# Kernel tuning notes

Hardware: AMD Instinct MI355X
Metric: run time of the kernel (lower is better)

The kernel has to match this reference:

```python
import jax, jax.numpy as jnp
import numpy as np

# sarModule stage: in=256, out=512, blocks=2, stride=2, patch_groups=4, mask_size=7
B, C_IN, H, W = 32, 256, 56, 56
C_OUT = 512
PLANES = C_OUT // 4   # Bottleneck inner width = planes // expansion = 128
G = 4                 # patch_groups
MS = 7                # mask_size
TEMP = 1.0            # gumbel-softmax temperature


def conv(x, w, stride=1, pad=0, groups=1):
    return jax.lax.conv_general_dilated(
        x, w, (stride, stride), [(pad, pad), (pad, pad)],
        feature_group_count=groups,
        dimension_numbers=('NCHW', 'OIHW', 'NCHW'))


def bn(x, g, b):
    # BatchNorm in inference form with running_mean=0, running_var=1 folded in
    return x * g[None, :, None, None] + b[None, :, None, None]


def avgpool3s2(x):
    # nn.AvgPool2d(3, stride=2, padding=1), count_include_pad=True
    s = jax.lax.reduce_window(x, 0.0, jax.lax.add, (1, 1, 3, 3), (1, 1, 2, 2),
                              [(0, 0), (0, 0), (1, 1), (1, 1)])
    return s / 9.0


def setup_inputs() -> dict:
    key = jax.random.key(0)
    ks = iter(jax.random.split(key, 64))

    def w(shape):
        fan_in = int(np.prod(shape[1:]))
        return jax.random.normal(next(ks), shape, jnp.float32) * np.float32((2.0 / fan_in) ** 0.5)

    ones = lambda n: jnp.ones((n,), jnp.float32)
    zeros = lambda n: jnp.zeros((n,), jnp.float32)

    x = jax.random.normal(next(ks), (B, C_IN, H, W), jnp.float32)
    u = jax.random.uniform(next(ks), (B, 2, G, MS, MS), jnp.float32, 1e-6, 1.0 - 1e-6)
    gumbel_noise = -jnp.log(-jnp.log(u))

    return dict(
        x=x, gumbel_noise=gumbel_noise,
        # base Bottleneck (256->512, stride 2, downsample = avgpool + 1x1 conv + bn)
        b_w1=w((PLANES, C_IN, 1, 1)), b_g1=ones(PLANES), b_b1=zeros(PLANES),
        b_w2=w((PLANES, PLANES, 3, 3)), b_g2=ones(PLANES), b_b2=zeros(PLANES),
        b_w3=w((C_OUT, PLANES, 1, 1)), b_g3=ones(C_OUT), b_b3=zeros(C_OUT),
        b_dw=w((C_OUT, C_IN, 1, 1)), b_dg=ones(C_OUT), b_db=zeros(C_OUT),
        # refine Bottleneck (256->512, stride 1, downsample = 1x1 conv + bn)
        r_w1=w((PLANES, C_IN, 1, 1)), r_g1=ones(PLANES), r_b1=zeros(PLANES),
        r_w2=w((PLANES, PLANES, 3, 3)), r_g2=ones(PLANES), r_b2=zeros(PLANES),
        r_w3=w((C_OUT, PLANES, 1, 1)), r_g3=ones(C_OUT), r_b3=zeros(C_OUT),
        r_dw=w((C_OUT, C_IN, 1, 1)), r_dg=ones(C_OUT), r_db=zeros(C_OUT),
        # maskGen: grouped 3x3 conv (512 -> 4*G), bn, pool, grouped 1x1 fc (4*G -> 2*G)
        m_w=w((4 * G, C_OUT // G, 3, 3)), m_g=ones(4 * G), m_b=zeros(4 * G),
        m_fcw=w((2 * G, 4, 1, 1)),
        m_fcb=jnp.concatenate([0.1 * ones(G), 5.0 * ones(G)]),  # bias init from maskGen
        # fusion Bottleneck (512->512, stride 2, downsample = avgpool only)
        f_w1=w((PLANES, C_OUT, 1, 1)), f_g1=ones(PLANES), f_b1=zeros(PLANES),
        f_w2=w((PLANES, PLANES, 3, 3)), f_g2=ones(PLANES), f_b2=zeros(PLANES),
        f_w3=w((C_OUT, PLANES, 1, 1)), f_g3=ones(C_OUT), f_b3=zeros(C_OUT),
    )


def reference(x, gumbel_noise,
              b_w1, b_g1, b_b1, b_w2, b_g2, b_b2, b_w3, b_g3, b_b3, b_dw, b_dg, b_db,
              r_w1, r_g1, r_b1, r_w2, r_g2, r_b2, r_w3, r_g3, r_b3, r_dw, r_dg, r_db,
              m_w, m_g, m_b, m_fcw, m_fcb,
              f_w1, f_g1, f_b1, f_w2, f_g2, f_b2, f_w3, f_g3, f_b3):
    # ---- base branch: Bottleneck stride 2, last_relu=False -> [B,512,28,28]
    o = jax.nn.relu(bn(conv(x, b_w1), b_g1, b_b1))
    o = jax.nn.relu(bn(conv(o, b_w2, stride=2, pad=1), b_g2, b_b2))
    o = bn(conv(o, b_w3), b_g3, b_b3)
    x_base = o + bn(conv(avgpool3s2(x), b_dw), b_dg, b_db)

    # ---- maskGen on x_base
    gmap = jax.nn.relu(bn(conv(x_base, m_w, pad=1, groups=G), m_g, m_b))      # [B,16,28,28]
    hb = x_base.shape[2] // MS                                                 # adaptive avgpool 28->7
    gmap = gmap.reshape(B, 4 * G, MS, hb, MS, hb).mean(axis=(3, 5))            # [B,16,7,7]
    logits = conv(gmap, m_fcw, groups=G) + m_fcb[None, :, None, None]          # [B,8,7,7]
    logits = logits.reshape(B, 2, G, MS, MS)                                   # view(B,2,groups,ms,ms)
    # hard gumbel-softmax over dim 1 with straight-through estimator
    y = jax.nn.softmax((logits + gumbel_noise) / TEMP, axis=1)
    hard = jax.nn.one_hot(jnp.argmax(y, axis=1), 2, axis=1, dtype=y.dtype)
    gates = hard + y - jax.lax.stop_gradient(y)
    mask = gates[:, 1]                                                         # [B,G,7,7]

    # nearest-upsample mask x8 and expand across each channel group
    mask_up = jnp.repeat(jnp.repeat(mask, H // MS, axis=-2), W // MS, axis=-1) # [B,G,56,56]
    mask_full = jnp.broadcast_to(mask_up[:, :, None], (B, G, C_OUT // G, H, W)).reshape(B, C_OUT, H, W)

    # ---- refine branch: Bottleneck stride 1, output gated by mask, last_relu=False
    o = jax.nn.relu(bn(conv(x, r_w1), r_g1, r_b1))
    o = jax.nn.relu(bn(conv(o, r_w2, pad=1), r_g2, r_b2))
    o = bn(conv(o, r_w3), r_g3, r_b3) * mask_full
    x_refine = o + bn(conv(x, r_dw), r_dg, r_db)                               # [B,512,56,56]

    # ---- fuse: bilinear upsample base to refine resolution (align_corners=False)
    x_base_up = jax.image.resize(x_base, (B, C_OUT, H, W), 'bilinear')
    fused = jax.nn.relu(x_base_up + x_refine)

    # ---- fusion Bottleneck: stride 2, downsample = avgpool only, last_relu=True
    o = jax.nn.relu(bn(conv(fused, f_w1), f_g1, f_b1))
    o = jax.nn.relu(bn(conv(o, f_w2, stride=2, pad=1), f_g2, f_b2))
    o = bn(conv(o, f_w3), f_g3, f_b3)
    out = jax.nn.relu(o + avgpool3s2(fused))                                   # [B,512,28,28]
    return out, mask
```

## Files before the change

kernel.cpp:

```cpp
#include <hip/hip_runtime.h>
#include <cstdint>

#define BB   32
#define CINX 256
#define HH   56
#define WW   56
#define HWX  3136
#define CO   512
#define PL   128
#define HP   28
#define WP   28
#define HWP  784
#define NG   4
#define MSZ  7

typedef unsigned short ushortT;
typedef unsigned int   uint32;
typedef __attribute__((ext_vector_type(8))) short short8;
typedef __attribute__((ext_vector_type(4))) float f32x4;

__device__ __forceinline__ ushortT f2bf(float f){
  uint32 u = __float_as_uint(f);
  u = (u + 0x7fffu + ((u >> 16) & 1u)) >> 16;
  return (ushortT)u;
}
__device__ __forceinline__ float bf2f(ushortT u){
  return __uint_as_float(((uint32)u) << 16);
}
__device__ __forceinline__ void split2(float v, ushortT& h, ushortT& lo){
  h = f2bf(v);
  lo = f2bf(v - bf2f(h));
}
__device__ __forceinline__ uint32 packu(ushortT a, ushortT b){
  return (uint32)a | ((uint32)b << 16);
}

__device__ __forceinline__ void wsplit(float v, ushortT* dh, ushortT* dl, size_t i){
  ushortT h, lo; split2(v, h, lo); dh[i] = h; dl[i] = lo;
}

__global__ __launch_bounds__(256) void prep_w(
  const float* __restrict__ b_w1, const float* __restrict__ b_g1,
  const float* __restrict__ b_w2, const float* __restrict__ b_g2,
  const float* __restrict__ b_w3, const float* __restrict__ b_g3,
  const float* __restrict__ b_dw, const float* __restrict__ b_dg,
  const float* __restrict__ r_w1, const float* __restrict__ r_g1,
  const float* __restrict__ r_w2, const float* __restrict__ r_g2,
  const float* __restrict__ r_w3, const float* __restrict__ r_g3,
  const float* __restrict__ r_dw, const float* __restrict__ r_dg,
  const float* __restrict__ f_w1, const float* __restrict__ f_g1,
  const float* __restrict__ f_w2, const float* __restrict__ f_g2,
  const float* __restrict__ f_w3, const float* __restrict__ f_g3,
  ushortT* __restrict__ dh, ushortT* __restrict__ dl)
{
  const int idx = blockIdx.x*256 + threadIdx.x;
  switch (blockIdx.y){
    case 0: {
      if (idx >= 32768) return; int m = idx >> 8;
      wsplit(b_w1[idx]*b_g1[m], dh, dl, (size_t)0 + idx); } break;
    case 1: {
      if (idx >= 147456) return; int m = idx / 1152; int k = idx - m*1152;
      int tap = k >> 7, c = k & 127;
      wsplit(b_w2[((size_t)(m*128 + c))*9 + tap]*b_g2[m], dh, dl, 32768 + (size_t)idx); } break;
    case 2: {
      if (idx >= 196608) return; int m = idx / 384; int k = idx - m*384;
      float v = (k < 128) ? b_w3[m*128 + k]*b_g3[m] : b_dw[m*256 + (k-128)]*b_dg[m];
      wsplit(v, dh, dl, 180224 + (size_t)idx); } break;
    case 3: {
      if (idx >= 32768) return; int m = idx >> 8;
      wsplit(r_w1[idx]*r_g1[m], dh, dl, 376832 + (size_t)idx); } break;
    case 4: {
      if (idx >= 147456) return; int m = idx / 1152; int k = idx - m*1152;
      int tap = k >> 7, c = k & 127;
      wsplit(r_w2[((size_t)(m*128 + c))*9 + tap]*r_g2[m], dh, dl, 409600 + (size_t)idx); } break;
    case 5: {
      if (idx >= 196608) return; int m = idx / 384; int k = idx - m*384;
      float v = (k < 128) ? r_w3[m*128 + k]*r_g3[m] : r_dw[m*256 + (k-128)]*r_dg[m];
      wsplit(v, dh, dl, 557056 + (size_t)idx); } break;
    case 6: {
      if (idx >= 65536) return; int m = idx >> 9;
      wsplit(f_w1[idx]*f_g1[m], dh, dl, 753664 + (size_t)idx); } break;
    case 7: {
      if (idx >= 147456) return; int m = idx / 1152; int k = idx - m*1152;
      int tap = k >> 7, c = k & 127;
      wsplit(f_w2[((size_t)(m*128 + c))*9 + tap]*f_g2[m], dh, dl, 819200 + (size_t)idx); } break;
    case 8: {
      if (idx >= 65536) return; int m = idx >> 7;
      wsplit(f_w3[idx]*f_g3[m], dh, dl, 966656 + (size_t)idx); } break;
  }
}

__global__ __launch_bounds__(256) void k_avgpool_x(const float* __restrict__ x, float* __restrict__ out){
  int idx = blockIdx.x*256 + threadIdx.x;
  if (idx >= BB*CINX*HWP) return;
  int p = idx % HWP; int bc = idx / HWP;
  int ox = p % WP, oy = p / WP;
  const float* src = x + (size_t)bc*HWX;
  float s = 0.f;
  #pragma unroll
  for (int dy=0; dy<3; dy++){
    int yy = 2*oy-1+dy;
    if ((unsigned)yy >= HH) continue;
    #pragma unroll
    for (int dx=0; dx<3; dx++){
      int xx = 2*ox-1+dx;
      if ((unsigned)xx >= WW) continue;
      s += src[yy*WW + xx];
    }
  }
  out[idx] = s * (1.f/9.f);
}

__global__ __launch_bounds__(256) void prep_p(const float* __restrict__ t,
    ushortT* __restrict__ ph_, ushortT* __restrict__ pl_){
  __shared__ float s[16][17];
  const int p0 = blockIdx.x*16, c0 = blockIdx.y*16, bz = blockIdx.z;
  const int ci = threadIdx.x >> 4, pi = threadIdx.x & 15;
  s[ci][pi] = t[((size_t)bz*CINX + c0 + ci)*HWP + p0 + pi];
  __syncthreads();
  const int pr = threadIdx.x >> 4, cj = threadIdx.x & 15;
  float v = s[cj][pr];
  ushortT h, lo; split2(v, h, lo);
  size_t o = ((size_t)bz*HWP + p0 + pr)*CINX + c0 + cj;
  ph_[o] = h; pl_[o] = lo;
}

__global__ __launch_bounds__(256) void k_poolf(const ushortT* __restrict__ fzh,
    const ushortT* __restrict__ fzl, float* __restrict__ pf){
  const int p = blockIdx.x, bz = blockIdx.y;
  const int oy = p / WP, ox = p - oy*WP;
  const int c = threadIdx.x*2;
  float s0 = 0.f, s1 = 0.f;
  #pragma unroll
  for (int dy=0; dy<3; dy++){
    const int iy = 2*oy - 1 + dy;
    if ((unsigned)iy >= (unsigned)HH) continue;
    #pragma unroll
    for (int dx=0; dx<3; dx++){
      const int ix = 2*ox - 1 + dx;
      if ((unsigned)ix >= (unsigned)WW) continue;
      const size_t fi = ((size_t)bz*HWX + (size_t)(iy*WW + ix))*CO + c;
      uint32 hh = *(const uint32*)(fzh + fi);
      uint32 ll = *(const uint32*)(fzl + fi);
      s0 += bf2f((ushortT)(hh & 0xffff)) + bf2f((ushortT)(ll & 0xffff));
      s1 += bf2f((ushortT)(hh >> 16))    + bf2f((ushortT)(ll >> 16));
    }
  }
  const size_t o = ((size_t)bz*HWP + p)*CO + c;
  pf[o]   = s0 * (1.f/9.f);
  pf[o+1] = s1 * (1.f/9.f);
}

template<int KIND,int EPI,int S1F,int S2F,int STRIDE,int PAD,int HIN,int WIN,
         int WOUT,int NOUT,int C1,int C2,int MTOT,int KTOT>
__global__ __launch_bounds__(256)
void gemm_bf3(const ushortT* __restrict__ wph, const ushortT* __restrict__ wpl,
              const ushortT* __restrict__ s1h, const ushortT* __restrict__ s1l,
              const ushortT* __restrict__ s2h, const ushortT* __restrict__ s2l,
              const float* __restrict__ xf32,
              const float* __restrict__ bias1, const float* __restrict__ bias2,
              const float* __restrict__ maskf, const float* __restrict__ xbase,
              ushortT* __restrict__ oh, ushortT* __restrict__ ol,
              float* __restrict__ of32)
{
  __shared__ ushortT smem[16384];
  ushortT* AH  = smem;
  ushortT* AL  = smem + 4096;
  ushortT* BHs = smem + 8192;
  ushortT* BLs = smem + 12288;

  const int tid = threadIdx.x;
  const int nt = blockIdx.x, mt = blockIdx.y, bz = blockIdx.z;
  const int l  = tid & 63, w = tid >> 6;
  const int wm = w >> 1, wn = w & 1;

  const int sr = tid >> 1;
  const int hp = tid & 1;
  const int swz = (sr >> 1) & 3;
  const int lws0 = sr*32 + ((2*hp) ^ swz)*8;
  const int lws1 = sr*32 + ((2*hp + 1) ^ swz)*8;

  const size_t arow = (size_t)(mt*128 + sr)*KTOT + hp*16;

  const int ng = nt*128 + sr;
  int oyS = 0, oxS = 0;
  if (KIND == 1){ oyS = ng / WOUT; oxS = ng - (ng / WOUT)*WOUT; }

  float mvstage = 1.f;
  if (KIND == 3){
    if (ng < NOUT){
      int yy = ng / WOUT, xx = ng - (ng / WOUT)*WOUT;
      mvstage = maskf[((size_t)(bz*NG + mt)*MSZ + (yy>>3))*MSZ + (xx>>3)];
    } else mvstage = 0.f;
  }

  f32x4 acc[4][4];
  f32x4 zf = {0.f,0.f,0.f,0.f};
  #pragma unroll
  for (int i=0;i<4;i++)
    #pragma unroll
    for (int j=0;j<4;j++) acc[i][j] = zf;

  const int NK = KTOT / 32;
  for (int ks=0; ks<NK; ks++){
    const int k0 = ks*32;
    uint4 a0 = *(const uint4*)(wph + arow + k0);
    uint4 a1 = *(const uint4*)(wph + arow + k0 + 8);
    uint4 a2 = *(const uint4*)(wpl + arow + k0);
    uint4 a3 = *(const uint4*)(wpl + arow + k0 + 8);
    uint4 b0 = make_uint4(0,0,0,0), b1v = b0, b2v = b0, b3v = b0;
    bool valid = false;
    bool usef = false;
    size_t brow = 0, fbase = 0;
    const ushortT* psh = s1h; const ushortT* psl = s1l;
    if (KIND == 0){
      valid = (ng < NOUT);
      if (S1F == 1){
        usef = true;
        fbase = ((size_t)bz*C1 + k0 + hp*16)*(size_t)NOUT + ng;
      } else {
        brow = ((size_t)bz*NOUT + ng)*C1 + k0 + hp*16;
      }
    } else if (KIND == 1){
      const int tap = k0 / C1;
      const int c   = k0 - tap*C1;
      const int dy = tap/3, dx = tap - 3*(tap/3);
      const int iy = oyS*STRIDE + dy - PAD;
      const int ix = oxS*STRIDE + dx - PAD;
      valid = (ng < NOUT) && (iy >= 0) && (iy < HIN) && (ix >= 0) && (ix < WIN);
      brow = ((size_t)bz*(HIN*WIN) + (size_t)(iy*WIN + ix))*C1 + c + hp*16;
    } else {
      valid = (ng < NOUT);
      if (k0 < C1){
        if (KIND == 3 && mvstage == 0.f) valid = false;
        brow = ((size_t)bz*NOUT + ng)*C1 + k0 + hp*16;
      } else {
        if (S2F == 1){
          usef = true;
          fbase = ((size_t)bz*C2 + (k0 - C1) + hp*16)*(size_t)NOUT + ng;
        } else {
          psh = s2h; psl = s2l;
          brow = ((size_t)bz*NOUT + ng)*C2 + (k0 - C1) + hp*16;
        }
      }
    }
    if (valid){
      if (usef){
        ushortT h[16], lo[16];
        #pragma unroll
        for (int e=0;e<16;e++){
          float v = xf32[fbase + (size_t)e*NOUT];
          split2(v, h[e], lo[e]);
        }
        b0  = make_uint4(packu(h[0],h[1]),  packu(h[2],h[3]),  packu(h[4],h[5]),  packu(h[6],h[7]));
        b1v = make_uint4(packu(h[8],h[9]),  packu(h[10],h[11]),packu(h[12],h[13]),packu(h[14],h[15]));
        b2v = make_uint4(packu(lo[0],lo[1]),packu(lo[2],lo[3]),packu(lo[4],lo[5]),packu(lo[6],lo[7]));
        b3v = make_uint4(packu(lo[8],lo[9]),packu(lo[10],lo[11]),packu(lo[12],lo[13]),packu(lo[14],lo[15]));
      } else {
        b0  = *(const uint4*)(psh + brow);
        b1v = *(const uint4*)(psh + brow + 8);
        b2v = *(const uint4*)(psl + brow);
        b3v = *(const uint4*)(psl + brow + 8);
      }
    }
    *(uint4*)(AH  + lws0) = a0;  *(uint4*)(AH  + lws1) = a1;
    *(uint4*)(AL  + lws0) = a2;  *(uint4*)(AL  + lws1) = a3;
    *(uint4*)(BHs + lws0) = b0;  *(uint4*)(BHs + lws1) = b1v;
    *(uint4*)(BLs + lws0) = b2v; *(uint4*)(BLs + lws1) = b3v;
    __syncthreads();

    short8 bh[4], bl[4];
    #pragma unroll
    for (int nf=0; nf<4; nf++){
      const int rr = wn*64 + nf*16 + (l & 15);
      const int ph = (l >> 4) ^ ((rr >> 1) & 3);
      bh[nf] = *(const short8*)(BHs + rr*32 + ph*8);
      bl[nf] = *(const short8*)(BLs + rr*32 + ph*8);
    }
    #pragma unroll
    for (int mf=0; mf<4; mf++){
      const int rr = wm*64 + mf*16 + (l & 15);
      const int ph = (l >> 4) ^ ((rr >> 1) & 3);
      short8 ah = *(const short8*)(AH + rr*32 + ph*8);
      short8 al = *(const short8*)(AL + rr*32 + ph*8);
      #pragma unroll
      for (int nf=0; nf<4; nf++)
        acc[mf][nf] = __builtin_amdgcn_mfma_f32_16x16x32_bf16(ah, bh[nf], acc[mf][nf], 0,0,0);
      #pragma unroll
      for (int nf=0; nf<4; nf++)
        acc[mf][nf] = __builtin_amdgcn_mfma_f32_16x16x32_bf16(ah, bl[nf], acc[mf][nf], 0,0,0);
      #pragma unroll
      for (int nf=0; nf<4; nf++)
        acc[mf][nf] = __builtin_amdgcn_mfma_f32_16x16x32_bf16(al, bh[nf], acc[mf][nf], 0,0,0);
    }
    __syncthreads();
  }

  const int mb0 = mt*128 + wm*64;
  const int nb0 = nt*128 + wn*64;

  #pragma unroll
  for (int nf=0; nf<4; nf++){
    const int n = nb0 + nf*16 + (l & 15);
    if (n >= NOUT) continue;
    if constexpr (EPI == 0){
      const size_t ob = ((size_t)bz*NOUT + n)*MTOT;
      #pragma unroll
      for (int mf=0; mf<4; mf++){
        const int m0 = mb0 + mf*16 + (l>>4)*4;
        ushort4 hq, lq; ushortT h0, l0; float v;
        v = fmaxf(acc[mf][nf][0] + bias1[m0+0], 0.f); split2(v,h0,l0); hq.x=h0; lq.x=l0;
        v = fmaxf(acc[mf][nf][1] + bias1[m0+1], 0.f); split2(v,h0,l0); hq.y=h0; lq.y=l0;
        v = fmaxf(acc[mf][nf][2] + bias1[m0+2], 0.f); split2(v,h0,l0); hq.z=h0; lq.z=l0;
        v = fmaxf(acc[mf][nf][3] + bias1[m0+3], 0.f); split2(v,h0,l0); hq.w=h0; lq.w=l0;
        *(ushort4*)(oh + ob + m0) = hq;
        *(ushort4*)(ol + ob + m0) = lq;
      }
    } else if constexpr (EPI == 1){
      #pragma unroll
      for (int mf=0; mf<4; mf++){
        const int m0 = mb0 + mf*16 + (l>>4)*4;
        #pragma unroll
        for (int r=0;r<4;r++){
          const int m = m0 + r;
          of32[((size_t)bz*MTOT + m)*NOUT + n] = acc[mf][nf][r] + bias1[m] + bias2[m];
        }
      }
    } else if constexpr (EPI == 2){
      const int y = n / WOUT, x = n - (n / WOUT)*WOUT;
      const float mvv = maskf[((size_t)(bz*NG + mt)*MSZ + (y>>3))*MSZ + (x>>3)];
      const int iy = y >> 1, ix = x >> 1;
      int yA,yB,xA,xB; float wyA,wyB,wxA,wxB;
      if (y & 1){ yA=iy; wyA=0.75f; yB=(iy+1<HP)?iy+1:HP-1; wyB=0.25f; }
      else      { yA=(iy>0)?iy-1:0; wyA=0.25f; yB=iy; wyB=0.75f; }
      if (x & 1){ xA=ix; wxA=0.75f; xB=(ix+1<WP)?ix+1:WP-1; wxB=0.25f; }
      else      { xA=(ix>0)?ix-1:0; wxA=0.25f; xB=ix; wxB=0.75f; }
      const size_t ob = ((size_t)bz*NOUT + n)*MTOT;
      #pragma unroll
      for (int mf=0; mf<4; mf++){
        const int m0 = mb0 + mf*16 + (l>>4)*4;
        ushort4 hq, lq;
        #pragma unroll
        for (int r=0;r<4;r++){
          const int m = m0 + r;
          const float* xb = xbase + ((size_t)bz*MTOT + m)*HWP;
          float up = wyA*(wxA*xb[yA*WP+xA] + wxB*xb[yA*WP+xB])
                   + wyB*(wxA*xb[yB*WP+xA] + wxB*xb[yB*WP+xB]);
          float v = fmaxf(acc[mf][nf][r] + up + mvv*bias1[m] + bias2[m], 0.f);
          ushortT h0, l0; split2(v, h0, l0);
          if      (r==0){hq.x=h0;lq.x=l0;}
          else if (r==1){hq.y=h0;lq.y=l0;}
          else if (r==2){hq.z=h0;lq.z=l0;}
          else          {hq.w=h0;lq.w=l0;}
        }
        *(ushort4*)(oh + ob + m0) = hq;
        *(ushort4*)(ol + ob + m0) = lq;
      }
    } else {
      const float* pfrow = xbase + ((size_t)bz*NOUT + n)*MTOT;
      #pragma unroll
      for (int mf=0; mf<4; mf++){
        const int m0 = mb0 + mf*16 + (l>>4)*4;
        const float4 pv = *(const float4*)(pfrow + m0);
        of32[((size_t)bz*MTOT + m0+0)*NOUT + n] = fmaxf(acc[mf][nf][0] + bias1[m0+0] + pv.x, 0.f);
        of32[((size_t)bz*MTOT + m0+1)*NOUT + n] = fmaxf(acc[mf][nf][1] + bias1[m0+1] + pv.y, 0.f);
        of32[((size_t)bz*MTOT + m0+2)*NOUT + n] = fmaxf(acc[mf][nf][2] + bias1[m0+2] + pv.z, 0.f);
        of32[((size_t)bz*MTOT + m0+3)*NOUT + n] = fmaxf(acc[mf][nf][3] + bias1[m0+3] + pv.w, 0.f);
      }
    }
  }
}

#define GM_LDSW 9216
__global__ __launch_bounds__(256) void k_gmap2(const float* __restrict__ xbase,
    const float* __restrict__ mw, const float* __restrict__ mg, const float* __restrict__ mb,
    float* __restrict__ gmap){
  __shared__ float wsh[GM_LDSW];
  __shared__ float red[16][2][4][16];
  const int tile = blockIdx.x, b = blockIdx.y;
  const int tid = threadIdx.x;
  const int pl = tid & 15, cs = tid >> 4;
  const int p = tile*16 + pl;
  const int oy = p / WP, ox = p - oy*WP;
  int toff[9];
  #pragma unroll
  for (int tap=0; tap<9; tap++){
    int dy = tap/3, dx = tap - 3*dy;
    int yy = oy + dy - 1, xx = ox + dx - 1;
    toff[tap] = ((unsigned)yy < (unsigned)HP && (unsigned)xx < (unsigned)WP) ? (yy*WP + xx) : -1;
  }
  float acc[2][4] = {{0.f,0.f,0.f,0.f},{0.f,0.f,0.f,0.f}};
  for (int pass=0; pass<2; pass++){
    __syncthreads();
    for (int i = tid; i < GM_LDSW; i += 256){
      int ocl = i & 3, tap = (i >> 2) % 9, c_rel = i / 36;
      int cg = pass*256 + c_rel;
      int g = cg >> 7;
      int oc = g*4 + ocl;
      wsh[i] = mw[((size_t)(oc*128 + (cg & 127)))*9 + tap] * mg[oc];
    }
    __syncthreads();
    const float* xb = xbase + ((size_t)b*CO + pass*256 + cs*16)*HWP;
    for (int cl=0; cl<16; cl++){
      const float* xc = xb + (size_t)cl*HWP;
      const float* wr = &wsh[(cs*16 + cl)*36];
      #pragma unroll
      for (int tap=0; tap<9; tap++){
        if (toff[tap] < 0) continue;
        float v = xc[toff[tap]];
        f32x4 w4 = *(const f32x4*)(wr + tap*4);
        acc[pass][0] += v*w4[0];
        acc[pass][1] += v*w4[1];
        acc[pass][2] += v*w4[2];
        acc[pass][3] += v*w4[3];
      }
    }
  }
  #pragma unroll
  for (int pp=0; pp<2; pp++)
    #pragma unroll
    for (int o=0; o<4; o++)
      red[cs][pp][o][pl] = acc[pp][o];
  __syncthreads();
  const int oc = tid >> 4;
  const int g = oc >> 2, ocl = oc & 3, pg = g >> 1, cs0 = (g & 1)*8;
  float s = 0.f;
  #pragma unroll
  for (int t=0; t<8; t++) s += red[cs0 + t][pg][ocl][pl];
  s = fmaxf(s + mb[oc], 0.f);
  gmap[((size_t)b*16 + oc)*HWP + p] = s;
}

__global__ __launch_bounds__(256) void k_gpool(const float* __restrict__ gmap, float* __restrict__ gpool){
  int idx = blockIdx.x*256 + threadIdx.x;
  if (idx >= BB*16*49) return;
  int q = idx % 49; int t = idx / 49; int ch = t % 16; int b = t / 16;
  int my = q/7, mx = q%7;
  const float* src = gmap + ((size_t)b*16 + ch)*HWP;
  float s = 0.f;
  #pragma unroll
  for (int yb=0;yb<4;yb++)
    #pragma unroll
    for (int xb=0;xb<4;xb++)
      s += src[(my*4+yb)*WP + (mx*4+xb)];
  gpool[idx] = s * (1.f/16.f);
}

__global__ __launch_bounds__(256) void k_mask(const float* __restrict__ gpool, const float* __restrict__ fcw,
    const float* __restrict__ fcb, const float* __restrict__ gum,
    float* __restrict__ maskf, float* __restrict__ mout){
  int idx = blockIdx.x*256 + threadIdx.x;
  if (idx >= BB*NG*49) return;
  int q = idx % 49; int t = idx / 49; int g = t % NG; int b = t / NG;
  float lgt[2];
  #pragma unroll
  for (int cls=0; cls<2; cls++){
    int c = cls*NG + g;
    int gc = c >> 1;
    float s = fcb[c];
    #pragma unroll
    for (int k=0;k<4;k++)
      s += fcw[c*4+k] * gpool[((size_t)b*16 + gc*4 + k)*49 + q];
    s += gum[(((size_t)b*2 + cls)*NG + g)*49 + q];
    lgt[cls] = s;
  }
  float m = (lgt[1] > lgt[0]) ? 1.f : 0.f;
  maskf[idx] = m;
  mout[idx] = m;
}

extern "C" void kernel_launch(void* const* d_in, const int* in_sizes, int n_in,
                              void* d_out, int out_size, void* d_ws, size_t ws_size,
                              hipStream_t stream){
  const float* x    = (const float*)d_in[0];
  const float* gum  = (const float*)d_in[1];
  const float* b_w1 = (const float*)d_in[2];
  const float* b_g1 = (const float*)d_in[3];
  const float* b_b1 = (const float*)d_in[4];
  const float* b_w2 = (const float*)d_in[5];
  const float* b_g2 = (const float*)d_in[6];
  const float* b_b2 = (const float*)d_in[7];
  const float* b_w3 = (const float*)d_in[8];
  const float* b_g3 = (const float*)d_in[9];
  const float* b_b3 = (const float*)d_in[10];
  const float* b_dw = (const float*)d_in[11];
  const float* b_dg = (const float*)d_in[12];
  const float* b_db = (const float*)d_in[13];
  const float* r_w1 = (const float*)d_in[14];
  const float* r_g1 = (const float*)d_in[15];
  const float* r_b1 = (const float*)d_in[16];
  const float* r_w2 = (const float*)d_in[17];
  const float* r_g2 = (const float*)d_in[18];
  const float* r_b2 = (const float*)d_in[19];
  const float* r_w3 = (const float*)d_in[20];
  const float* r_g3 = (const float*)d_in[21];
  const float* r_b3 = (const float*)d_in[22];
  const float* r_dw = (const float*)d_in[23];
  const float* r_dg = (const float*)d_in[24];
  const float* r_db = (const float*)d_in[25];
  const float* m_w  = (const float*)d_in[26];
  const float* m_g  = (const float*)d_in[27];
  const float* m_b  = (const float*)d_in[28];
  const float* m_fcw= (const float*)d_in[29];
  const float* m_fcb= (const float*)d_in[30];
  const float* f_w1 = (const float*)d_in[31];
  const float* f_g1 = (const float*)d_in[32];
  const float* f_b1 = (const float*)d_in[33];
  const float* f_w2 = (const float*)d_in[34];
  const float* f_g2 = (const float*)d_in[35];
  const float* f_b2 = (const float*)d_in[36];
  const float* f_w3 = (const float*)d_in[37];
  const float* f_g3 = (const float*)d_in[38];
  const float* f_b3 = (const float*)d_in[39];

  char* ws = (char*)d_ws;
  constexpr size_t O_WPH  = 0;
  constexpr size_t O_WPL  = 2064384;
  constexpr size_t O_CH   = 4128768;
  constexpr size_t O_CL   = 29818880;
  constexpr size_t O_DH   = 55508992;
  constexpr size_t O_DL   = 61931520;
  constexpr size_t O_EH   = 68354048;
  constexpr size_t O_EL   = 94044160;
  constexpr size_t O_PF   = O_EH;
  constexpr size_t O_XB   = 119734272;
  constexpr size_t O_GMAP = 171114496;
  constexpr size_t O_GPOOL= 172720128;
  constexpr size_t O_MASK = 172820480;
  constexpr size_t O_FH   = 172845568;
  constexpr size_t O_PH   = 172845568;
  constexpr size_t O_PL   = 185690624;
  constexpr size_t O_FL   = 275606016;

  ushortT* WPH = (ushortT*)(ws + O_WPH);
  ushortT* WPL = (ushortT*)(ws + O_WPL);
  ushortT* CHp = (ushortT*)(ws + O_CH);
  ushortT* CLp = (ushortT*)(ws + O_CL);
  ushortT* DHp = (ushortT*)(ws + O_DH);
  ushortT* DLp = (ushortT*)(ws + O_DL);
  ushortT* EHp = (ushortT*)(ws + O_EH);
  ushortT* ELp = (ushortT*)(ws + O_EL);
  float*   PF  = (float*)(ws + O_PF);
  float*   XB  = (float*)(ws + O_XB);
  float*   PTMP= (float*)(ws + O_XB);
  ushortT* PHp = (ushortT*)(ws + O_PH);
  ushortT* PLp = (ushortT*)(ws + O_PL);
  ushortT* FHp = (ushortT*)(ws + O_FH);
  ushortT* FLp = (ushortT*)(ws + O_FL);
  float*   GMAP = (float*)(ws + O_GMAP);
  float*   GPOOL= (float*)(ws + O_GPOOL);
  float*   MASKF= (float*)(ws + O_MASK);
  (void)ws_size;

  float* outp = (float*)d_out;
  float* mout = outp + (size_t)BB*CO*HWP;

  dim3 blk(256);
  const ushortT* nu = nullptr; const float* nf_ = nullptr;
  ushortT* nuo = nullptr; float* nfo = nullptr;

  prep_w<<<dim3(768, 9), blk, 0, stream>>>(b_w1,b_g1,b_w2,b_g2,b_w3,b_g3,b_dw,b_dg,
      r_w1,r_g1,r_w2,r_g2,r_w3,r_g3,r_dw,r_dg,f_w1,f_g1,f_w2,f_g2,f_w3,f_g3, WPH, WPL);
  k_avgpool_x<<<dim3((BB*CINX*HWP+255)/256), blk, 0, stream>>>(x, PTMP);
  prep_p<<<dim3(49, 16, BB), blk, 0, stream>>>(PTMP, PHp, PLp);

  gemm_bf3<0,0,1,0,1,0,56,56,56,3136,256,0,128,256><<<dim3(25,1,BB), blk, 0, stream>>>(
      WPH+0, WPL+0, nu, nu, nu, nu, x, b_b1, nf_, nf_, nf_, CHp, CLp, nfo);
  gemm_bf3<1,0,0,0,2,1,56,56,28,784,128,0,128,1152><<<dim3(7,1,BB), blk, 0, stream>>>(
      WPH+32768, WPL+32768, CHp, CLp, nu, nu, nf_, b_b2, nf_, nf_, nf_, DHp, DLp, nfo);
  gemm_bf3<2,1,0,0,1,0,28,28,28,784,128,256,512,384><<<dim3(7,4,BB), blk, 0, stream>>>(
      WPH+180224, WPL+180224, DHp, DLp, PHp, PLp, nf_, b_b3, b_db, nf_, nf_, nuo, nuo, XB);

  k_gmap2<<<dim3(49, BB), blk, 0, stream>>>(XB, m_w, m_g, m_b, GMAP);
  k_gpool<<<dim3(98), blk, 0, stream>>>(GMAP, GPOOL);
  k_mask<<<dim3(25), blk, 0, stream>>>(GPOOL, m_fcw, m_fcb, gum, MASKF, mout);

  gemm_bf3<0,0,1,0,1,0,56,56,56,3136,256,0,128,256><<<dim3(25,1,BB), blk, 0, stream>>>(
      WPH+376832, WPL+376832, nu, nu, nu, nu, x, r_b1, nf_, nf_, nf_, CHp, CLp, nfo);
  gemm_bf3<1,0,0,0,1,1,56,56,56,3136,128,0,128,1152><<<dim3(25,1,BB), blk, 0, stream>>>(
      WPH+409600, WPL+409600, CHp, CLp, nu, nu, nf_, r_b2, nf_, nf_, nf_, EHp, ELp, nfo);
  gemm_bf3<3,2,0,1,1,0,56,56,56,3136,128,256,512,384><<<dim3(25,4,BB), blk, 0, stream>>>(
      WPH+557056, WPL+557056, EHp, ELp, nu, nu, x, r_b3, r_db, MASKF, XB, FHp, FLp, nfo);

  k_poolf<<<dim3(HWP, BB), blk, 0, stream>>>(FHp, FLp, PF);

  gemm_bf3<0,0,0,0,1,0,56,56,56,3136,512,0,128,512><<<dim3(25,1,BB), blk, 0, stream>>>(
      WPH+753664, WPL+753664, FHp, FLp, nu, nu, nf_, f_b1, nf_, nf_, nf_, CHp, CLp, nfo);
  gemm_bf3<1,0,0,0,2,1,56,56,28,784,128,0,128,1152><<<dim3(7,1,BB), blk, 0, stream>>>(
      WPH+819200, WPL+819200, CHp, CLp, nu, nu, nf_, f_b2, nf_, nf_, nf_, DHp, DLp, nfo);
  gemm_bf3<0,3,0,0,1,0,28,28,28,784,128,0,512,128><<<dim3(7,4,BB), blk, 0, stream>>>(
      WPH+966656, WPL+966656, DHp, DLp, nu, nu, nf_, f_b3, nf_, nf_, PF, nuo, nuo, outp);
}
```

Baseline: 1.119 ms.

## Use direct global-to-LDS loads, merge first 1x1 convs, add 256-row tiles

Replaces register-staged global loads of the weight and activation tiles with global_load_lds direct-to-LDS transfers, using a zero page for out-of-bounds rows. Both first 1x1 convs of the base and refine branches now run as one GEMM with 256 output rows over x, stored interleaved with row stride 256. Some GEMMs use a 256-row M tile with 512 threads. The aim is to cut VGPR staging and duplicate reads of x, at the cost of extra LDS, buffers placed in the output region as scratch, and more template complexity.

```diff
diff --git a/kernel.cpp b/kernel.cpp
--- a/kernel.cpp
+++ b/kernel.cpp
@@ -35,6 +35,12 @@
   return (uint32)a | ((uint32)b << 16);
 }
 
+typedef __attribute__((address_space(1))) const void g_void;
+typedef __attribute__((address_space(3))) void l_void;
+__device__ __forceinline__ void glds16(const ushortT* g, ushortT* l){
+  __builtin_amdgcn_global_load_lds((g_void*)g, (l_void*)l, 16, 0, 0);
+}
+
 __device__ __forceinline__ void wsplit(float v, ushortT* dh, ushortT* dl, size_t i){
   ushortT h, lo; split2(v, h, lo); dh[i] = h; dl[i] = lo;
 }
@@ -51,24 +57,26 @@
   const float* __restrict__ f_w1, const float* __restrict__ f_g1,
   const float* __restrict__ f_w2, const float* __restrict__ f_g2,
   const float* __restrict__ f_w3, const float* __restrict__ f_g3,
-  ushortT* __restrict__ dh, ushortT* __restrict__ dl)
+  const float* __restrict__ b_b1, const float* __restrict__ r_b1,
+  ushortT* __restrict__ dh, ushortT* __restrict__ dl,
+  ushortT* __restrict__ zp, float* __restrict__ biasC)
 {
   const int idx = blockIdx.x*256 + threadIdx.x;
   switch (blockIdx.y){
     case 0: {
       if (idx >= 32768) return; int m = idx >> 8;
       wsplit(b_w1[idx]*b_g1[m], dh, dl, (size_t)0 + idx); } break;
+    case 3: {
+      if (idx >= 32768) return; int m = idx >> 8;
+      wsplit(r_w1[idx]*r_g1[m], dh, dl, 32768 + (size_t)idx); } break;
     case 1: {
       if (idx >= 147456) return; int m = idx / 1152; int k = idx - m*1152;
       int tap = k >> 7, c = k & 127;
-      wsplit(b_w2[((size_t)(m*128 + c))*9 + tap]*b_g2[m], dh, dl, 32768 + (size_t)idx); } break;
+      wsplit(b_w2[((size_t)(m*128 + c))*9 + tap]*b_g2[m], dh, dl, 65536 + (size_t)idx); } break;
     case 2: {
       if (idx >= 196608) return; int m = idx / 384; int k = idx - m*384;
       float v = (k < 128) ? b_w3[m*128 + k]*b_g3[m] : b_dw[m*256 + (k-128)]*b_dg[m];
-      wsplit(v, dh, dl, 180224 + (size_t)idx); } break;
-    case 3: {
-      if (idx >= 32768) return; int m = idx >> 8;
-      wsplit(r_w1[idx]*r_g1[m], dh, dl, 376832 + (size_t)idx); } break;
+      wsplit(v, dh, dl, 212992 + (size_t)idx); } break;
     case 4: {
       if (idx >= 147456) return; int m = idx / 1152; int k = idx - m*1152;
       int tap = k >> 7, c = k & 127;
@@ -87,6 +95,11 @@
     case 8: {
       if (idx >= 65536) return; int m = idx >> 7;
       wsplit(f_w3[idx]*f_g3[m], dh, dl, 966656 + (size_t)idx); } break;
+    case 9: {
+      if (idx < 64) zp[idx] = 0;
+      if (idx < 128) biasC[idx] = b_b1[idx];
+      else if (idx < 256) biasC[idx] = r_b1[idx-128];
+    } break;
   }
 }
 
@@ -151,48 +164,70 @@
   pf[o+1] = s1 * (1.f/9.f);
 }
 
-template<int KIND,int EPI,int S1F,int S2F,int STRIDE,int PAD,int HIN,int WIN,
-         int WOUT,int NOUT,int C1,int C2,int MTOT,int KTOT>
-__global__ __launch_bounds__(256)
+template<int KIND,int EPI,int S1F,int S2F,int MT,int STRIDE,int PAD,int HIN,int WIN,
+         int WOUT,int NOUT,int C1,int C2,int BSTR1,int MTOT,int KTOT>
+__global__ __launch_bounds__(MT*2)
 void gemm_bf3(const ushortT* __restrict__ wph, const ushortT* __restrict__ wpl,
               const ushortT* __restrict__ s1h, const ushortT* __restrict__ s1l,
               const ushortT* __restrict__ s2h, const ushortT* __restrict__ s2l,
               const float* __restrict__ xf32,
               const float* __restrict__ bias1, const float* __restrict__ bias2,
               const float* __restrict__ maskf, const float* __restrict__ xbase,
+              const ushortT* __restrict__ zp,
               ushortT* __restrict__ oh, ushortT* __restrict__ ol,
               float* __restrict__ of32)
 {
-  __shared__ ushortT smem[16384];
+  constexpr int NW = MT/32;
+  constexpr int BCALLS = 8/NW;
+  constexpr bool GATHER1 = (KIND==0 && S1F==1);
+  constexpr bool GATHER2 = (KIND>=2 && S2F==1);
+  __shared__ ushortT smem[MT*64 + 8192];
   ushortT* AH  = smem;
-  ushortT* AL  = smem + 4096;
-  ushortT* BHs = smem + 8192;
-  ushortT* BLs = smem + 12288;
+  ushortT* AL  = smem + MT*32;
+  ushortT* BHs = smem + MT*64;
+  ushortT* BLs = smem + MT*64 + 4096;
 
   const int tid = threadIdx.x;
   const int nt = blockIdx.x, mt = blockIdx.y, bz = blockIdx.z;
   const int l  = tid & 63, w = tid >> 6;
   const int wm = w >> 1, wn = w & 1;
+
+  size_t a_src[2]; int a_dst[2];
+  #pragma unroll
+  for (int c=0;c<2;c++){
+    int s = (w*2 + c)*64 + l;
+    int row = s >> 2, slotm = s & 3;
+    int logical = slotm ^ ((row >> 1) & 3);
+    a_src[c] = (size_t)(mt*MT + row)*KTOT + logical*8;
+    a_dst[c] = (w*2 + c)*512;
+  }
+
+  int b_dst[2]; size_t b_base1[2], b_base2[2]; int b_klane[2];
+  int b_oy[2], b_ox[2]; bool b_ok[2]; float b_mv[2];
+  #pragma unroll
+  for (int c=0;c<BCALLS;c++){
+    int s = (w*BCALLS + c)*64 + l;
+    int row = s >> 2, slotm = s & 3;
+    int logical = slotm ^ ((row >> 1) & 3);
+    b_klane[c] = logical*8;
+    b_dst[c] = (w*BCALLS + c)*512;
+    int ngr = nt*128 + row;
+    b_ok[c] = (ngr < NOUT);
+    int oyv = ngr / WOUT, oxv = ngr - (ngr / WOUT)*WOUT;
+    b_oy[c] = oyv; b_ox[c] = oxv;
+    b_base1[c] = ((size_t)bz*NOUT + ngr)*BSTR1 + b_klane[c];
+    b_base2[c] = ((size_t)bz*NOUT + ngr)*C2 + b_klane[c];
+    b_mv[c] = 1.f;
+    if (KIND == 3)
+      b_mv[c] = b_ok[c] ? maskf[((size_t)(bz*NG + mt)*MSZ + (oyv>>3))*MSZ + (oxv>>3)] : 0.f;
+  }
 
   const int sr = tid >> 1;
   const int hp = tid & 1;
   const int swz = (sr >> 1) & 3;
   const int lws0 = sr*32 + ((2*hp) ^ swz)*8;
   const int lws1 = sr*32 + ((2*hp + 1) ^ swz)*8;
-
-  const size_t arow = (size_t)(mt*128 + sr)*KTOT + hp*16;
-
   const int ng = nt*128 + sr;
-  int oyS = 0, oxS = 0;
-  if (KIND == 1){ oyS = ng / WOUT; oxS = ng - (ng / WOUT)*WOUT; }
-
-  float mvstage = 1.f;
-  if (KIND == 3){
-    if (ng < NOUT){
-      int yy = ng / WOUT, xx = ng - (ng / WOUT)*WOUT;
-      mvstage = maskf[((size_t)(bz*NG + mt)*MSZ + (yy>>3))*MSZ + (xx>>3)];
-    } else mvstage = 0.f;
-  }
 
   f32x4 acc[4][4];
   f32x4 zf = {0.f,0.f,0.f,0.f};
@@ -204,69 +239,75 @@
   const int NK = KTOT / 32;
   for (int ks=0; ks<NK; ks++){
     const int k0 = ks*32;
-    uint4 a0 = *(const uint4*)(wph + arow + k0);
-    uint4 a1 = *(const uint4*)(wph + arow + k0 + 8);
-    uint4 a2 = *(const uint4*)(wpl + arow + k0);
-    uint4 a3 = *(const uint4*)(wpl + arow + k0 + 8);
-    uint4 b0 = make_uint4(0,0,0,0), b1v = b0, b2v = b0, b3v = b0;
-    bool valid = false;
-    bool usef = false;
-    size_t brow = 0, fbase = 0;
-    const ushortT* psh = s1h; const ushortT* psl = s1l;
-    if (KIND == 0){
-      valid = (ng < NOUT);
-      if (S1F == 1){
-        usef = true;
-        fbase = ((size_t)bz*C1 + k0 + hp*16)*(size_t)NOUT + ng;
-      } else {
-        brow = ((size_t)bz*NOUT + ng)*C1 + k0 + hp*16;
-      }
-    } else if (KIND == 1){
-      const int tap = k0 / C1;
-      const int c   = k0 - tap*C1;
-      const int dy = tap/3, dx = tap - 3*(tap/3);
-      const int iy = oyS*STRIDE + dy - PAD;
-      const int ix = oxS*STRIDE + dx - PAD;
-      valid = (ng < NOUT) && (iy >= 0) && (iy < HIN) && (ix >= 0) && (ix < WIN);
-      brow = ((size_t)bz*(HIN*WIN) + (size_t)(iy*WIN + ix))*C1 + c + hp*16;
+    #pragma unroll
+    for (int c=0;c<2;c++){
+      glds16(wph + a_src[c] + k0, AH + a_dst[c]);
+      glds16(wpl + a_src[c] + k0, AL + a_dst[c]);
+    }
+    if constexpr (GATHER1){
+      if (tid < 256){
+        uint4 b0 = make_uint4(0,0,0,0), b1v = b0, b2v = b0, b3v = b0;
+        if (ng < NOUT){
+          size_t fbase = ((size_t)bz*C1 + k0 + hp*16)*(size_t)NOUT + ng;
+          ushortT h[16], lo[16];
+          #pragma unroll
+          for (int e=0;e<16;e++){ split2(xf32[fbase + (size_t)e*NOUT], h[e], lo[e]); }
+          b0  = make_uint4(packu(h[0],h[1]),  packu(h[2],h[3]),  packu(h[4],h[5]),  packu(h[6],h[7]));
+          b1v = make_uint4(packu(h[8],h[9]),  packu(h[10],h[11]),packu(h[12],h[13]),packu(h[14],h[15]));
+          b2v = make_uint4(packu(lo[0],lo[1]),packu(lo[2],lo[3]),packu(lo[4],lo[5]),packu(lo[6],lo[7]));
+          b3v = make_uint4(packu(lo[8],lo[9]),packu(lo[10],lo[11]),packu(lo[12],lo[13]),packu(lo[14],lo[15]));
+        }
+        *(uint4*)(BHs + lws0) = b0;  *(uint4*)(BHs + lws1) = b1v;
+        *(uint4*)(BLs + lws0) = b2v; *(uint4*)(BLs + lws1) = b3v;
+      }
+    } else if (GATHER2 && k0 >= C1){
+      if (tid < 256){
+        uint4 b0 = make_uint4(0,0,0,0), b1v = b0, b2v = b0, b3v = b0;
+        if (ng < NOUT){
+          size_t fbase = ((size_t)bz*C2 + (k0 - C1) + hp*16)*(size_t)NOUT + ng;
+          ushortT h[16], lo[16];
+          #pragma unroll
+          for (int e=0;e<16;e++){ split2(xf32[fbase + (size_t)e*NOUT], h[e], lo[e]); }
+          b0  = make_uint4(packu(h[0],h[1]),  packu(h[2],h[3]),  packu(h[4],h[5]),  packu(h[6],h[7]));
+          b1v = make_uint4(packu(h[8],h[9]),  packu(h[10],h[11]),packu(h[12],h[13]),packu(h[14],h[15]));
+          b2v = make_uint4(packu(lo[0],lo[1]),packu(lo[2],lo[3]),packu(lo[4],lo[5]),packu(lo[6],lo[7]));
+          b3v = make_uint4(packu(lo[8],lo[9]),packu(lo[10],lo[11]),packu(lo[12],lo[13]),packu(lo[14],lo[15]));
+        }
+        *(uint4*)(BHs + lws0) = b0;  *(uint4*)(BHs + lws1) = b1v;
+        *(uint4*)(BLs + lws0) = b2v; *(uint4*)(BLs + lws1) = b3v;
+      }
     } else {
-      valid = (ng < NOUT);
-      if (k0 < C1){
-        if (KIND == 3 && mvstage == 0.f) valid = false;
-        brow = ((size_t)bz*NOUT + ng)*C1 + k0 + hp*16;
-      } else {
-        if (S2F == 1){
-          usef = true;
-          fbase = ((size_t)bz*C2 + (k0 - C1) + hp*16)*(size_t)NOUT + ng;
+      #pragma unroll
+      for (int c=0;c<BCALLS;c++){
+        const ushortT *sh, *sl;
+        if constexpr (KIND == 0){
+          bool ok = b_ok[c];
+          size_t off = b_base1[c] + k0;
+          sh = ok ? s1h + off : zp;  sl = ok ? s1l + off : zp;
+        } else if constexpr (KIND == 1){
+          const int tap = k0 >> 7;
+          const int cb  = (k0 & 127);
+          const int dy = tap/3, dx = tap - 3*(tap/3);
+          int iy = b_oy[c]*STRIDE + dy - PAD;
+          int ix = b_ox[c]*STRIDE + dx - PAD;
+          bool ok = b_ok[c] && (unsigned)iy < (unsigned)HIN && (unsigned)ix < (unsigned)WIN;
+          size_t off = ((size_t)bz*(HIN*WIN) + (size_t)(iy*WIN + ix))*BSTR1 + cb + b_klane[c];
+          sh = ok ? s1h + off : zp;  sl = ok ? s1l + off : zp;
         } else {
-          psh = s2h; psl = s2l;
-          brow = ((size_t)bz*NOUT + ng)*C2 + (k0 - C1) + hp*16;
+          if (k0 < C1){
+            bool ok = b_ok[c] && (KIND != 3 || b_mv[c] != 0.f);
+            size_t off = b_base1[c] + k0;
+            sh = ok ? s1h + off : zp;  sl = ok ? s1l + off : zp;
+          } else {
+            bool ok = b_ok[c];
+            size_t off = b_base2[c] + (k0 - C1);
+            sh = ok ? s2h + off : zp;  sl = ok ? s2l + off : zp;
+          }
         }
-      }
-    }
-    if (valid){
-      if (usef){
-        ushortT h[16], lo[16];
-        #pragma unroll
-        for (int e=0;e<16;e++){
-          float v = xf32[fbase + (size_t)e*NOUT];
-          split2(v, h[e], lo[e]);
-        }
-        b0  = make_uint4(packu(h[0],h[1]),  packu(h[2],h[3]),  packu(h[4],h[5]),  packu(h[6],h[7]));
-        b1v = make_uint4(packu(h[8],h[9]),  packu(h[10],h[11]),packu(h[12],h[13]),packu(h[14],h[15]));
-        b2v = make_uint4(packu(lo[0],lo[1]),packu(lo[2],lo[3]),packu(lo[4],lo[5]),packu(lo[6],lo[7]));
-        b3v = make_uint4(packu(lo[8],lo[9]),packu(lo[10],lo[11]),packu(lo[12],lo[13]),packu(lo[14],lo[15]));
-      } else {
-        b0  = *(const uint4*)(psh + brow);
-        b1v = *(const uint4*)(psh + brow + 8);
-        b2v = *(const uint4*)(psl + brow);
-        b3v = *(const uint4*)(psl + brow + 8);
-      }
-    }
-    *(uint4*)(AH  + lws0) = a0;  *(uint4*)(AH  + lws1) = a1;
-    *(uint4*)(AL  + lws0) = a2;  *(uint4*)(AL  + lws1) = a3;
-    *(uint4*)(BHs + lws0) = b0;  *(uint4*)(BHs + lws1) = b1v;
-    *(uint4*)(BLs + lws0) = b2v; *(uint4*)(BLs + lws1) = b3v;
+        glds16(sh, BHs + b_dst[c]);
+        glds16(sl, BLs + b_dst[c]);
+      }
+    }
     __syncthreads();
 
     short8 bh[4], bl[4];
@@ -296,7 +337,7 @@
     __syncthreads();
   }
 
-  const int mb0 = mt*128 + wm*64;
+  const int mb0 = mt*MT + wm*64;
   const int nb0 = nt*128 + wn*64;
 
   #pragma unroll
@@ -328,7 +369,8 @@
       }
     } else if constexpr (EPI == 2){
       const int y = n / WOUT, x = n - (n / WOUT)*WOUT;
-      const float mvv = maskf[((size_t)(bz*NG + mt)*MSZ + (y>>3))*MSZ + (x>>3)];
+      const int grpw = (mt*MT + wm*64) >> 7;
+      const float mvv = maskf[((size_t)(bz*NG + grpw)*MSZ + (y>>3))*MSZ + (x>>3)];
       const int iy = y >> 1, ix = x >> 1;
       int yA,yB,xA,xB; float wyA,wyB,wxA,wxB;
       if (y & 1){ yA=iy; wyA=0.75f; yB=(iy+1<HP)?iy+1:HP-1; wyB=0.25f; }
@@ -517,7 +559,6 @@
   constexpr size_t O_WPH  = 0;
   constexpr size_t O_WPL  = 2064384;
   constexpr size_t O_CH   = 4128768;
-  constexpr size_t O_CL   = 29818880;
   constexpr size_t O_DH   = 55508992;
   constexpr size_t O_DL   = 61931520;
   constexpr size_t O_EH   = 68354048;
@@ -531,11 +572,14 @@
   constexpr size_t O_PH   = 172845568;
   constexpr size_t O_PL   = 185690624;
   constexpr size_t O_FL   = 275606016;
+  constexpr size_t O_ZP   = 378366464;
+  constexpr size_t O_BIASC= 378366592;
 
   ushortT* WPH = (ushortT*)(ws + O_WPH);
   ushortT* WPL = (ushortT*)(ws + O_WPL);
-  ushortT* CHp = (ushortT*)(ws + O_CH);
-  ushortT* CLp = (ushortT*)(ws + O_CL);
+  ushortT* MGH = (ushortT*)(ws + O_CH);
+  ushortT* F1H = (ushortT*)(ws + O_CH);
+  ushortT* F1L = (ushortT*)(ws + O_CH + 25690112);
   ushortT* DHp = (ushortT*)(ws + O_DH);
   ushortT* DLp = (ushortT*)(ws + O_DL);
   ushortT* EHp = (ushortT*)(ws + O_EH);
@@ -550,44 +594,46 @@
   float*   GMAP = (float*)(ws + O_GMAP);
   float*   GPOOL= (float*)(ws + O_GPOOL);
   float*   MASKF= (float*)(ws + O_MASK);
+  ushortT* ZP  = (ushortT*)(ws + O_ZP);
+  float*   BIASC = (float*)(ws + O_BIASC);
   (void)ws_size;
 
   float* outp = (float*)d_out;
   float* mout = outp + (size_t)BB*CO*HWP;
-
-  dim3 blk(256);
+  ushortT* dout_u = (ushortT*)d_out;
+
+  dim3 blk(256), blk2(512);
   const ushortT* nu = nullptr; const float* nf_ = nullptr;
   ushortT* nuo = nullptr; float* nfo = nullptr;
 
-  prep_w<<<dim3(768, 9), blk, 0, stream>>>(b_w1,b_g1,b_w2,b_g2,b_w3,b_g3,b_dw,b_dg,
-      r_w1,r_g1,r_w2,r_g2,r_w3,r_g3,r_dw,r_dg,f_w1,f_g1,f_w2,f_g2,f_w3,f_g3, WPH, WPL);
+  prep_w<<<dim3(768, 10), blk, 0, stream>>>(b_w1,b_g1,b_w2,b_g2,b_w3,b_g3,b_dw,b_dg,
+      r_w1,r_g1,r_w2,r_g2,r_w3,r_g3,r_dw,r_dg,f_w1,f_g1,f_w2,f_g2,f_w3,f_g3,
+      b_b1, r_b1, WPH, WPL, ZP, BIASC);
   k_avgpool_x<<<dim3((BB*CINX*HWP+255)/256), blk, 0, stream>>>(x, PTMP);
   prep_p<<<dim3(49, 16, BB), blk, 0, stream>>>(PTMP, PHp, PLp);
 
-  gemm_bf3<0,0,1,0,1,0,56,56,56,3136,256,0,128,256><<<dim3(25,1,BB), blk, 0, stream>>>(
-      WPH+0, WPL+0, nu, nu, nu, nu, x, b_b1, nf_, nf_, nf_, CHp, CLp, nfo);
-  gemm_bf3<1,0,0,0,2,1,56,56,28,784,128,0,128,1152><<<dim3(7,1,BB), blk, 0, stream>>>(
-      WPH+32768, WPL+32768, CHp, CLp, nu, nu, nf_, b_b2, nf_, nf_, nf_, DHp, DLp, nfo);
-  gemm_bf3<2,1,0,0,1,0,28,28,28,784,128,256,512,384><<<dim3(7,4,BB), blk, 0, stream>>>(
-      WPH+180224, WPL+180224, DHp, DLp, PHp, PLp, nf_, b_b3, b_db, nf_, nf_, nuo, nuo, XB);
+  gemm_bf3<0,0,1,0,256, 1,0,56,56,56,3136, 256,0,256, 256,256><<<dim3(25,1,BB), blk2, 0, stream>>>(
+      WPH+0, WPL+0, nu, nu, nu, nu, x, BIASC, nf_, nf_, nf_, ZP, MGH, dout_u, nfo);
+  gemm_bf3<1,0,0,0,128, 2,1,56,56,28,784, 128,0,256, 128,1152><<<dim3(7,1,BB), blk, 0, stream>>>(
+      WPH+65536, WPL+65536, MGH, dout_u, nu, nu, nf_, b_b2, nf_, nf_, nf_, ZP, DHp, DLp, nfo);
+  gemm_bf3<2,1,0,0,256, 1,0,28,28,28,784, 128,256,128, 512,384><<<dim3(7,2,BB), blk2, 0, stream>>>(
+      WPH+212992, WPL+212992, DHp, DLp, PHp, PLp, nf_, b_b3, b_db, nf_, nf_, ZP, nuo, nuo, XB);
 
   k_gmap2<<<dim3(49, BB), blk, 0, stream>>>(XB, m_w, m_g, m_b, GMAP);
   k_gpool<<<dim3(98), blk, 0, stream>>>(GMAP, GPOOL);
   k_mask<<<dim3(25), blk, 0, stream>>>(GPOOL, m_fcw, m_fcb, gum, MASKF, mout);
 
-  gemm_bf3<0,0,1,0,1,0,56,56,56,3136,256,0,128,256><<<dim3(25,1,BB), blk, 0, stream>>>(
-      WPH+376832, WPL+376832, nu, nu, nu, nu, x, r_b1, nf_, nf_, nf_, CHp, CLp, nfo);
-  gemm_bf3<1,0,0,0,1,1,56,56,56,3136,128,0,128,1152><<<dim3(25,1,BB), blk, 0, stream>>>(
-      WPH+409600, WPL+409600, CHp, CLp, nu, nu, nf_, r_b2, nf_, nf_, nf_, EHp, ELp, nfo);
-  gemm_bf3<3,2,0,1,1,0,56,56,56,3136,128,256,512,384><<<dim3(25,4,BB), blk, 0, stream>>>(
-      WPH+557056, WPL+557056, EHp, ELp, nu, nu, x, r_b3, r_db, MASKF, XB, FHp, FLp, nfo);
+  gemm_bf3<1,0,0,0,128, 1,1,56,56,56,3136, 128,0,256, 128,1152><<<dim3(25,1,BB), blk, 0, stream>>>(
+      WPH+409600, WPL+409600, MGH+128, dout_u+128, nu, nu, nf_, r_b2, nf_, nf_, nf_, ZP, EHp, ELp, nfo);
+  gemm_bf3<3,2,0,1,128, 1,0,56,56,56,3136, 128,256,128, 512,384><<<dim3(25,4,BB), blk, 0, stream>>>(
+      WPH+557056, WPL+557056, EHp, ELp, nu, nu, x, r_b3, r_db, MASKF, XB, ZP, FHp, FLp, nfo);
 
   k_poolf<<<dim3(HWP, BB), blk, 0, stream>>>(FHp, FLp, PF);
 
-  gemm_bf3<0,0,0,0,1,0,56,56,56,3136,512,0,128,512><<<dim3(25,1,BB), blk, 0, stream>>>(
-      WPH+753664, WPL+753664, FHp, FLp, nu, nu, nf_, f_b1, nf_, nf_, nf_, CHp, CLp, nfo);
-  gemm_bf3<1,0,0,0,2,1,56,56,28,784,128,0,128,1152><<<dim3(7,1,BB), blk, 0, stream>>>(
-      WPH+819200, WPL+819200, CHp, CLp, nu, nu, nf_, f_b2, nf_, nf_, nf_, DHp, DLp, nfo);
-  gemm_bf3<0,3,0,0,1,0,28,28,28,784,128,0,512,128><<<dim3(7,4,BB), blk, 0, stream>>>(
-      WPH+966656, WPL+966656, DHp, DLp, nu, nu, nf_, f_b3, nf_, nf_, PF, nuo, nuo, outp);
-}
+  gemm_bf3<0,0,0,0,128, 1,0,56,56,56,3136, 512,0,512, 128,512><<<dim3(25,1,BB), blk, 0, stream>>>(
+      WPH+753664, WPL+753664, FHp, FLp, nu, nu, nf_, f_b1, nf_, nf_, nf_, ZP, F1H, F1L, nfo);
+  gemm_bf3<1,0,0,0,128, 2,1,56,56,28,784, 128,0,128, 128,1152><<<dim3(7,1,BB), blk, 0, stream>>>(
+      WPH+819200, WPL+819200, F1H, F1L, nu, nu, nf_, f_b2, nf_, nf_, nf_, ZP, DHp, DLp, nfo);
+  gemm_bf3<0,3,0,0,256, 1,0,28,28,28,784, 128,0,128, 512,128><<<dim3(7,2,BB), blk2, 0, stream>>>(
+      WPH+966656, WPL+966656, DHp, DLp, nu, nu, nf_, f_b3, nf_, nf_, PF, ZP, nuo, nuo, outp);
+}
```

Result: no change. 1.104 ms (-1.3%).
